# Kernel optimization log

Hardware: AMD Instinct MI355X
Metric: run time of the kernel (lower is better)

The kernel has to match this reference:

```python
import jax, jax.numpy as jnp
import numpy as np

N = 50000      # nodes
E = 800000     # edges (avg degree 16)
IN = 128       # in_dim == hidden_dim*num_heads so residuals fire
D = 32         # hidden_dim (per-head)
H = 4          # num_heads
OUT = 64       # out_dim (final layer has 1 head)
NEG_SLOPE = 0.2
LN_EPS = 1e-5


def setup_inputs() -> dict:
    key = jax.random.key(0)
    ks = jax.random.split(key, 16)
    rn = lambda k, s: jax.random.normal(k, s, jnp.float32) * 0.05
    return {
        "features": jax.random.normal(ks[0], (N, IN), jnp.float32),
        "edge_weight": jax.random.uniform(ks[1], (E,), jnp.float32),
        "src": jax.random.randint(ks[2], (E,), 0, N),
        "dst": jax.random.randint(ks[3], (E,), 0, N),
        "W0": rn(ks[4], (IN, H * D)), "al0": rn(ks[5], (H, D)), "ar0": rn(ks[6], (H, D)), "lam0": jnp.float32(1.0),
        "W1": rn(ks[7], (H * D, H * D)), "al1": rn(ks[8], (H, D)), "ar1": rn(ks[9], (H, D)), "lam1": jnp.float32(1.0),
        "W2": rn(ks[10], (H * D, OUT)), "al2": rn(ks[11], (1, OUT)), "ar2": rn(ks[12], (1, OUT)), "lam2": jnp.float32(1.0),
        "g0": jnp.ones((H * D,), jnp.float32), "b0": jnp.zeros((H * D,), jnp.float32),
        "g1": jnp.ones((H * D,), jnp.float32), "b1": jnp.zeros((H * D,), jnp.float32),
    }


def _gat_layer(h, W, al, ar, lam, src, dst, ew):
    n = h.shape[0]
    heads, d = al.shape
    ft = (h @ W).reshape(n, heads, d)                      # [N,H,D]
    el = jnp.sum(ft * al[None], axis=-1)                   # [N,H]
    er = jnp.sum(ft * ar[None], axis=-1)                   # [N,H]
    e = el[src] + er[dst] + lam * ew[:, None]              # [E,H] u_add_v + weight bias
    e = jax.nn.leaky_relu(e, NEG_SLOPE)
    # edge softmax over incoming edges of each dst node
    m = jax.ops.segment_max(e, dst, num_segments=n)        # [N,H]
    ex = jnp.exp(e - m[dst])
    s = jax.ops.segment_sum(ex, dst, num_segments=n)       # [N,H]
    a = ex / s[dst]                                        # [E,H]
    # u_mul_e + sum aggregation
    msg = ft[src] * a[:, :, None]                          # [E,H,D]
    return jax.ops.segment_sum(msg, dst, num_segments=n)   # [N,H,D]


def _layer_norm(x, g, b):
    mu = jnp.mean(x, axis=-1, keepdims=True)
    var = jnp.mean((x - mu) ** 2, axis=-1, keepdims=True)
    return (x - mu) * jax.lax.rsqrt(var + LN_EPS) * g + b


def _forward(features, edge_weight, src, dst,
             W0, al0, ar0, lam0, W1, al1, ar1, lam1, W2, al2, ar2, lam2,
             g0, b0, g1, b1):
    n = features.shape[0]
    h = features
    # layer 0
    h1 = _gat_layer(h, W0, al0, ar0, lam0, src, dst, edge_weight)
    h1 = jax.nn.elu(h1).reshape(n, -1)
    h1 = _layer_norm(h1, g0, b0)
    if h1.shape == h.shape:
        h1 = h1 + h
    # layer 1
    h2 = _gat_layer(h1, W1, al1, ar1, lam1, src, dst, edge_weight)
    h2 = jax.nn.elu(h2).reshape(n, -1)
    h2 = _layer_norm(h2, g1, b1)
    h2 = h2 + h1
    # layer 2 (single head, no activation)
    out = _gat_layer(h2, W2, al2, ar2, lam2, src, dst, edge_weight).reshape(n, -1)
    return out


def reference(features, edge_weight, src, dst,
              W0, al0, ar0, lam0, W1, al1, ar1, lam1, W2, al2, ar2, lam2,
              g0, b0, g1, b1):
    # eval mode: dropout off and _add_noise is identity, so noisy == clean
    h_clean = _forward(features, edge_weight, src, dst,
                       W0, al0, ar0, lam0, W1, al1, ar1, lam1, W2, al2, ar2, lam2,
                       g0, b0, g1, b1)
    return (h_clean, h_clean)
```

## Files before the change

### kernel.cpp

```cpp
#include <hip/hip_runtime.h>

#define NEG_SLOPE 0.2f
#define LN_EPS 1e-5f

typedef __attribute__((ext_vector_type(8))) short bf16x8;
typedef __attribute__((ext_vector_type(4))) float f32x4;

__device__ inline unsigned short f2bf(float f) {
    unsigned u = __float_as_uint(f);
    unsigned r = u + 0x7FFFu + ((u >> 16) & 1u);
    return (unsigned short)(r >> 16);
}

__device__ inline void unpack8(uint4 u, float* f) {
    f[0] = __uint_as_float(u.x << 16);
    f[1] = __uint_as_float(u.x & 0xFFFF0000u);
    f[2] = __uint_as_float(u.y << 16);
    f[3] = __uint_as_float(u.y & 0xFFFF0000u);
    f[4] = __uint_as_float(u.z << 16);
    f[5] = __uint_as_float(u.z & 0xFFFF0000u);
    f[6] = __uint_as_float(u.w << 16);
    f[7] = __uint_as_float(u.w & 0xFFFF0000u);
}


__global__ void prep_kernel(const int* __restrict__ dst, int* __restrict__ counts,
                            int* __restrict__ rank, int E, int RB,
                            const float* __restrict__ W0, const float* __restrict__ W1,
                            const float* __restrict__ W2, unsigned short* __restrict__ Wt0,
                            unsigned short* __restrict__ Wt1,
                            unsigned short* __restrict__ Wt2) {
    int bid = blockIdx.x;
    if (bid < RB) {
        int i = bid * 256 + threadIdx.x;
        if (i < E) rank[i] = atomicAdd(&counts[dst[i] * 16], 1);
    } else {
        int row = (bid - RB) * 2 + (threadIdx.x >> 7);
        int k = threadIdx.x & 127;
        if (row < 128) {
            Wt0[row * 128 + k] = f2bf(W0[k * 128 + row]);
        } else if (row < 256) {
            int c = row - 128;
            Wt1[c * 128 + k] = f2bf(W1[k * 128 + c]);
        } else {
            int c = row - 256;
            Wt2[c * 128 + k] = f2bf(W2[k * 64 + c]);
        }
    }
}

__global__ __launch_bounds__(256) void scan1_kernel(const int* __restrict__ counts,
                                                    int* __restrict__ bsum,
                                                    int* __restrict__ dhist, int n) {
    __shared__ int lds[256];
    __shared__ int hbin[64];
    int t = threadIdx.x;
    if (t < 64) hbin[t] = 0;
    int i = blockIdx.x * 256 + t;
    int c = (i < n) ? counts[i * 16] : 0;
    lds[t] = c;
    __syncthreads();
    if (i < n) atomicAdd(&hbin[63 - (c < 63 ? c : 63)], 1);
    for (int off = 128; off > 0; off >>= 1) {
        int v = (t < off) ? lds[t + off] : 0;
        __syncthreads();
        if (t < off) lds[t] += v;
        __syncthreads();
    }
    if (t == 0) bsum[blockIdx.x] = lds[0];
    if (t < 64) {
        int h = hbin[t];
        if (h) atomicAdd(&dhist[t], h);
    }
}

__global__ __launch_bounds__(256) void scan3_kernel(const int* __restrict__ counts,
                                                    const int* __restrict__ bsum,
                                                    int* __restrict__ rowptr,
                                                    const int* __restrict__ dhist,
                                                    int* __restrict__ dbase,
                                                    int n, int E, int nscan) {
    __shared__ int lds[256];
    int t = threadIdx.x;
    lds[t] = (t < nscan) ? bsum[t] : 0;
    __syncthreads();
    for (int off = 1; off < 256; off <<= 1) {
        int v = (t >= off) ? lds[t - off] : 0;
        __syncthreads();
        lds[t] += v;
        __syncthreads();
    }
    int boff = (blockIdx.x > 0) ? lds[blockIdx.x - 1] : 0;
    __syncthreads();
    int i = blockIdx.x * 256 + t;
    int c = (i < n) ? counts[i * 16] : 0;
    lds[t] = c;
    __syncthreads();
    for (int off = 1; off < 256; off <<= 1) {
        int v = (t >= off) ? lds[t - off] : 0;
        __syncthreads();
        lds[t] += v;
        __syncthreads();
    }
    if (i < n) rowptr[i] = boff + lds[t] - c;
    if (i == n) rowptr[n] = E;
    if (blockIdx.x == 0 && t < 64) {
        int v = dhist[t];
        int x = v;
        #pragma unroll
        for (int off = 1; off < 64; off <<= 1) {
            int u = __shfl_up(x, off, 64);
            if (t >= off) x += u;
        }
        dbase[t] = x - v;
    }
}

__global__ __launch_bounds__(256) void place_kernel(
    const int* __restrict__ src, const int* __restrict__ dst,
    const float* __restrict__ ew, const int* __restrict__ rowptr,
    const int* __restrict__ rank, unsigned* __restrict__ edge_p,
    const int* __restrict__ dbase, int* __restrict__ dcount,
    int* __restrict__ perm, int E, int EB, int N) {
    __shared__ int lbin[64];
    __shared__ int lbase[64];
    int bid = blockIdx.x;
    int t = threadIdx.x;
    if (bid < EB) {
        int i = bid * 256 + t;
        if (i < E) {
            int p = rowptr[dst[i]] + rank[i];
            edge_p[p] = ((unsigned)f2bf(ew[i]) << 16) | (unsigned)src[i];
        }
    } else {
        if (t < 64) lbin[t] = 0;
        __syncthreads();
        int nidx = (bid - EB) * 256 + t;
        bool valid = nidx < N;
        int key = 0, myoff = 0;
        if (valid) {
            int deg = rowptr[nidx + 1] - rowptr[nidx];
            key = 63 - (deg < 63 ? deg : 63);
            myoff = atomicAdd(&lbin[key], 1);
        }
        __syncthreads();
        if (t < 64) lbase[t] = lbin[t] ? atomicAdd(&dcount[t], lbin[t]) : 0;
        __syncthreads();
        if (valid) perm[dbase[key] + lbase[key] + myoff] = nidx;
    }
}


template <int NT, int H, bool A32>
__global__ __launch_bounds__(256) void gemm_mfma(const void* __restrict__ Ap,
                                                 const unsigned short* __restrict__ Wt,
                                                 const float* __restrict__ al,
                                                 const float* __restrict__ ar,
                                                 unsigned short* __restrict__ ftb,
                                                 float* __restrict__ el,
                                                 float* __restrict__ er, int n) {
    constexpr int LDA = 136;
    constexpr int D = NT * 16 / H;
    __shared__ unsigned short As[64 * LDA];
    __shared__ unsigned short Ws[NT * 16 * LDA];
    int t = threadIdx.x;
    int row0 = blockIdx.x * 64;

    if constexpr (A32) {
        const float4* A4 = (const float4*)Ap;
        #pragma unroll
        for (int j = 0; j < 8; ++j) {
            int idx = t + j * 256;
            int r = idx >> 5;
            int c4 = idx & 31;
            int row = row0 + r;
            float4 v = (row < n) ? A4[(size_t)row * 32 + c4] : make_float4(0.f, 0.f, 0.f, 0.f);
            unsigned p0 = (unsigned)f2bf(v.x) | ((unsigned)f2bf(v.y) << 16);
            unsigned p1 = (unsigned)f2bf(v.z) | ((unsigned)f2bf(v.w) << 16);
            *(uint2*)&As[r * LDA + c4 * 4] = make_uint2(p0, p1);
        }
    } else {
        const uint4* A16 = (const uint4*)Ap;
        #pragma unroll
        for (int j = 0; j < 4; ++j) {
            int idx = t + j * 256;
            int r = idx >> 4;
            int c8 = idx & 15;
            int row = row0 + r;
            uint4 v = (row < n) ? A16[(size_t)row * 16 + c8] : make_uint4(0, 0, 0, 0);
            *(uint4*)&As[r * LDA + c8 * 8] = v;
        }
    }
    const uint4* Wg = (const uint4*)Wt;
    #pragma unroll
    for (int j = 0; j < NT; ++j) {
        int idx = t + j * 256;
        int r = idx >> 4;
        int c8 = idx & 15;
        *(uint4*)&Ws[r * LDA + c8 * 8] = Wg[idx];
    }
    __syncthreads();

    int w = t >> 6, lane = t & 63;
    int m = lane & 15, q = lane >> 4;
    f32x4 acc[NT] = {};
    const unsigned short* ap = &As[(w * 16 + m) * LDA + q * 8];
    #pragma unroll
    for (int kk = 0; kk < 4; ++kk) {
        bf16x8 a = *(const bf16x8*)(ap + kk * 32);
        #pragma unroll
        for (int nt = 0; nt < NT; ++nt) {
            bf16x8 b = *(const bf16x8*)&Ws[(nt * 16 + m) * LDA + kk * 32 + q * 8];
            acc[nt] = __builtin_amdgcn_mfma_f32_16x16x32_bf16(a, b, acc[nt], 0, 0, 0);
        }
    }

    float alv[NT], arv[NT];
    #pragma unroll
    for (int nt = 0; nt < NT; ++nt) {
        alv[nt] = al[nt * 16 + m];
        arv[nt] = ar[nt * 16 + m];
    }

    int orow = row0 + w * 16 + q * 4;
    #pragma unroll
    for (int r = 0; r < 4; ++r) {
        int row = orow + r;
        float pl[H] = {}, pr[H] = {};
        #pragma unroll
        for (int nt = 0; nt < NT; ++nt) {
            int h = (nt * 16) / D;
            pl[h] = fmaf(acc[nt][r], alv[nt], pl[h]);
            pr[h] = fmaf(acc[nt][r], arv[nt], pr[h]);
        }
        #pragma unroll
        for (int off = 1; off < 16; off <<= 1) {
            #pragma unroll
            for (int h = 0; h < H; ++h) {
                pl[h] += __shfl_xor(pl[h], off, 64);
                pr[h] += __shfl_xor(pr[h], off, 64);
            }
        }
        if (row < n) {
            #pragma unroll
            for (int nt = 0; nt < NT; ++nt)
                ftb[(size_t)row * (NT * 16) + nt * 16 + m] = f2bf(acc[nt][r]);
            if (m < H) {
                float vl = pl[0], vr = pr[0];
                #pragma unroll
                for (int h = 1; h < H; ++h)
                    if (m == h) { vl = pl[h]; vr = pr[h]; }
                el[row * H + m] = vl;
                er[row * H + m] = vr;
            }
        }
    }
}


__device__ inline void accum8(float* ax, uint4 u, float p) {
    ax[0] = fmaf(p, __uint_as_float(u.x << 16), ax[0]);
    ax[1] = fmaf(p, __uint_as_float(u.x & 0xFFFF0000u), ax[1]);
    ax[2] = fmaf(p, __uint_as_float(u.y << 16), ax[2]);
    ax[3] = fmaf(p, __uint_as_float(u.y & 0xFFFF0000u), ax[3]);
    ax[4] = fmaf(p, __uint_as_float(u.z << 16), ax[4]);
    ax[5] = fmaf(p, __uint_as_float(u.z & 0xFFFF0000u), ax[5]);
    ax[6] = fmaf(p, __uint_as_float(u.w << 16), ax[6]);
    ax[7] = fmaf(p, __uint_as_float(u.w & 0xFFFF0000u), ax[7]);
}

__device__ inline void accum4(float* ax, uint2 u, float p) {
    ax[0] = fmaf(p, __uint_as_float(u.x << 16), ax[0]);
    ax[1] = fmaf(p, __uint_as_float(u.x & 0xFFFF0000u), ax[1]);
    ax[2] = fmaf(p, __uint_as_float(u.y << 16), ax[2]);
    ax[3] = fmaf(p, __uint_as_float(u.y & 0xFFFF0000u), ax[3]);
}

template <int K>
__device__ inline void agg_batch(const uint4* __restrict__ ftb4,
                                 const float* __restrict__ el, unsigned ev, int j,
                                 int li, int head, float erv, float lam, float* ax,
                                 float& s) {
    unsigned ee[K];
    uint4 uu[K];
    float ll[K];
    #pragma unroll
    for (int k = 0; k < K; ++k) ee[k] = __shfl(ev, j + k, 16);
    #pragma unroll
    for (int k = 0; k < K; ++k) {
        unsigned sn = ee[k] & 0xFFFFu;
        uu[k] = ftb4[(size_t)sn * 16 + li];
        ll[k] = el[sn * 4 + head];
    }
    #pragma unroll
    for (int k = 0; k < K; ++k) {
        float v = ll[k] + erv + lam * __uint_as_float(ee[k] & 0xFFFF0000u);
        v = fmaxf(v, NEG_SLOPE * v);
        float p = __expf(v);
        accum8(ax, uu[k], p);
        s += p;
    }
}

template <int K>
__device__ inline void agg_batch_out(const uint2* __restrict__ ftb2,
                                     const float* __restrict__ el, unsigned ev,
                                     int j, int li, float erv, float lam, float* ax,
                                     float& s) {
    unsigned ee[K];
    uint2 uu[K];
    float ll[K];
    #pragma unroll
    for (int k = 0; k < K; ++k) ee[k] = __shfl(ev, j + k, 16);
    #pragma unroll
    for (int k = 0; k < K; ++k) {
        unsigned sn = ee[k] & 0xFFFFu;
        uu[k] = ftb2[(size_t)sn * 16 + li];
        ll[k] = el[sn];
    }
    #pragma unroll
    for (int k = 0; k < K; ++k) {
        float v = ll[k] + erv + lam * __uint_as_float(ee[k] & 0xFFFF0000u);
        v = fmaxf(v, NEG_SLOPE * v);
        float p = __expf(v);
        accum4(ax, uu[k], p);
        s += p;
    }
}

template <bool PREV32>
__global__ __launch_bounds__(256) void gat_agg_ln(
    const int* __restrict__ rowptr, const unsigned* __restrict__ edge_p,
    const int* __restrict__ perm, const uint4* __restrict__ ftb4,
    const float* __restrict__ el, const float* __restrict__ er,
    const float* __restrict__ lam_p, const float* __restrict__ g,
    const float* __restrict__ b, const void* __restrict__ prevp,
    uint4* __restrict__ outb, int n) {
    int gid = blockIdx.x * 16 + (threadIdx.x >> 4);
    if (gid >= n) return;
    int node = perm[gid];
    int li = threadIdx.x & 15;
    int head = li >> 2;
    float lam = lam_p[0];
    float erv = er[node * 4 + head];
    int s0 = rowptr[node], s1 = rowptr[node + 1];
    float ax[8] = {};
    float s = 0.f;

    for (int base = s0; base < s1; base += 16) {
        int m = s1 - base;
        if (m > 16) m = 16;
        unsigned ev = (li < m) ? edge_p[base + li] : 0u;
        int j = 0;
        for (; j + 8 <= m; j += 8)
            agg_batch<8>(ftb4, el, ev, j, li, head, erv, lam, ax, s);
        if (j + 4 <= m) {
            agg_batch<4>(ftb4, el, ev, j, li, head, erv, lam, ax, s);
            j += 4;
        }
        for (; j < m; ++j)
            agg_batch<1>(ftb4, el, ev, j, li, head, erv, lam, ax, s);
    }

    float inv = (s > 0.f) ? 1.f / s : 0.f;
    float x[8];
    float sum = 0.f, sq = 0.f;
    #pragma unroll
    for (int d = 0; d < 8; ++d) {
        float v = ax[d] * inv;
        v = (v > 0.f) ? v : expm1f(v);
        x[d] = v;
        sum += v;
        sq += v * v;
    }
    #pragma unroll
    for (int off = 1; off < 16; off <<= 1) {
        sum += __shfl_xor(sum, off, 16);
        sq += __shfl_xor(sq, off, 16);
    }
    float mu = sum * (1.f / 128.f);
    float var = sq * (1.f / 128.f) - mu * mu;
    float rs = rsqrtf(var + LN_EPS);

    const float4* g4 = (const float4*)g;
    const float4* b4 = (const float4*)b;
    float pv[8];
    if constexpr (PREV32) {
        const float4* p4 = (const float4*)prevp;
        #pragma unroll
        for (int h = 0; h < 2; ++h) {
            float4 v = p4[(size_t)node * 32 + li * 2 + h];
            pv[h * 4 + 0] = v.x; pv[h * 4 + 1] = v.y;
            pv[h * 4 + 2] = v.z; pv[h * 4 + 3] = v.w;
        }
    } else {
        unpack8(((const uint4*)prevp)[(size_t)node * 16 + li], pv);
    }
    float y[8];
    #pragma unroll
    for (int h = 0; h < 2; ++h) {
        float4 gv = g4[li * 2 + h];
        float4 bv = b4[li * 2 + h];
        y[h * 4 + 0] = (x[h * 4 + 0] - mu) * rs * gv.x + bv.x + pv[h * 4 + 0];
        y[h * 4 + 1] = (x[h * 4 + 1] - mu) * rs * gv.y + bv.y + pv[h * 4 + 1];
        y[h * 4 + 2] = (x[h * 4 + 2] - mu) * rs * gv.z + bv.z + pv[h * 4 + 2];
        y[h * 4 + 3] = (x[h * 4 + 3] - mu) * rs * gv.w + bv.w + pv[h * 4 + 3];
    }
    uint4 o;
    o.x = (unsigned)f2bf(y[0]) | ((unsigned)f2bf(y[1]) << 16);
    o.y = (unsigned)f2bf(y[2]) | ((unsigned)f2bf(y[3]) << 16);
    o.z = (unsigned)f2bf(y[4]) | ((unsigned)f2bf(y[5]) << 16);
    o.w = (unsigned)f2bf(y[6]) | ((unsigned)f2bf(y[7]) << 16);
    outb[(size_t)node * 16 + li] = o;
}

__global__ __launch_bounds__(256) void gat_agg_out(
    const int* __restrict__ rowptr, const unsigned* __restrict__ edge_p,
    const int* __restrict__ perm, const uint2* __restrict__ ftb2,
    const float* __restrict__ el, const float* __restrict__ er,
    const float* __restrict__ lam_p, float* __restrict__ out, int n) {
    int gid = blockIdx.x * 16 + (threadIdx.x >> 4);
    if (gid >= n) return;
    int node = perm[gid];
    int li = threadIdx.x & 15;
    float lam = lam_p[0];
    float erv = er[node];
    int s0 = rowptr[node], s1 = rowptr[node + 1];
    float ax[4] = {};
    float s = 0.f;

    for (int base = s0; base < s1; base += 16) {
        int m = s1 - base;
        if (m > 16) m = 16;
        unsigned ev = (li < m) ? edge_p[base + li] : 0u;
        int j = 0;
        for (; j + 8 <= m; j += 8)
            agg_batch_out<8>(ftb2, el, ev, j, li, erv, lam, ax, s);
        if (j + 4 <= m) {
            agg_batch_out<4>(ftb2, el, ev, j, li, erv, lam, ax, s);
            j += 4;
        }
        for (; j < m; ++j)
            agg_batch_out<1>(ftb2, el, ev, j, li, erv, lam, ax, s);
    }

    float inv = (s > 0.f) ? 1.f / s : 0.f;
    float4 y;
    y.x = ax[0] * inv;
    y.y = ax[1] * inv;
    y.z = ax[2] * inv;
    y.w = ax[3] * inv;
    ((float4*)out)[(size_t)node * 16 + li] = y;
    ((float4*)out)[(size_t)(n + node) * 16 + li] = y;
}


extern "C" void kernel_launch(void* const* d_in, const int* in_sizes, int n_in,
                              void* d_out, int out_size, void* d_ws, size_t ws_size,
                              hipStream_t stream) {
    const float* features = (const float*)d_in[0];
    const float* edge_weight = (const float*)d_in[1];
    const int* src = (const int*)d_in[2];
    const int* dst = (const int*)d_in[3];
    const float* W0 = (const float*)d_in[4];
    const float* al0 = (const float*)d_in[5];
    const float* ar0 = (const float*)d_in[6];
    const float* lam0 = (const float*)d_in[7];
    const float* W1 = (const float*)d_in[8];
    const float* al1 = (const float*)d_in[9];
    const float* ar1 = (const float*)d_in[10];
    const float* lam1 = (const float*)d_in[11];
    const float* W2 = (const float*)d_in[12];
    const float* al2 = (const float*)d_in[13];
    const float* ar2 = (const float*)d_in[14];
    const float* lam2 = (const float*)d_in[15];
    const float* g0 = (const float*)d_in[16];
    const float* b0 = (const float*)d_in[17];
    const float* g1 = (const float*)d_in[18];
    const float* b1 = (const float*)d_in[19];

    const int N = in_sizes[0] / 128;
    const int E = in_sizes[1];

    char* w = (char*)d_ws;
    size_t o = 0;
    auto carve = [&](size_t bytes) {
        char* p = w + o;
        o += (bytes + 255) & ~(size_t)255;
        return p;
    };
    int* counts = (int*)carve((size_t)N * 64);
    int* dhist = (int*)carve(256);
    int* dcount = (int*)carve(256);
    int* rowptr = (int*)carve((size_t)(N + 1) * 4);
    int* bsum = (int*)carve(256 * 4);
    int* rank = (int*)carve((size_t)E * 4);
    unsigned* edge_p = (unsigned*)carve((size_t)E * 4);
    int* dbase = (int*)carve(256);
    int* perm = (int*)carve((size_t)N * 4);
    unsigned short* ftb = (unsigned short*)carve((size_t)N * 128 * 2);
    unsigned short* h1 = (unsigned short*)carve((size_t)N * 128 * 2);
    unsigned short* h2 = (unsigned short*)carve((size_t)N * 128 * 2);
    float* el = (float*)carve((size_t)N * 4 * 4);
    float* er = (float*)carve((size_t)N * 4 * 4);
    unsigned short* Wt0 = (unsigned short*)carve(128 * 128 * 2);
    unsigned short* Wt1 = (unsigned short*)carve(128 * 128 * 2);
    unsigned short* Wt2 = (unsigned short*)carve(64 * 128 * 2);

    const int nscan = (N + 255) / 256;
    const int ngemm = (N + 63) / 64;
    const int nagg = (N + 15) / 16;
    const int RB = (E + 255) / 256;

    hipMemsetAsync(counts, 0, (size_t)N * 64 + 512, stream);
    prep_kernel<<<RB + 160, 256, 0, stream>>>(dst, counts, rank, E, RB,
                                              W0, W1, W2, Wt0, Wt1, Wt2);
    scan1_kernel<<<nscan, 256, 0, stream>>>(counts, bsum, dhist, N);
    scan3_kernel<<<(N + 1 + 255) / 256, 256, 0, stream>>>(counts, bsum, rowptr,
                                                          dhist, dbase, N, E, nscan);
    place_kernel<<<RB + nscan, 256, 0, stream>>>(src, dst, edge_weight, rowptr, rank,
                                                 edge_p, dbase, dcount, perm, E, RB, N);

    gemm_mfma<8, 4, true><<<ngemm, 256, 0, stream>>>(features, Wt0, al0, ar0,
                                                     ftb, el, er, N);
    gat_agg_ln<true><<<nagg, 256, 0, stream>>>(rowptr, edge_p, perm, (const uint4*)ftb,
                                               el, er, lam0, g0, b0, features,
                                               (uint4*)h1, N);
    gemm_mfma<8, 4, false><<<ngemm, 256, 0, stream>>>(h1, Wt1, al1, ar1, ftb, el, er, N);
    gat_agg_ln<false><<<nagg, 256, 0, stream>>>(rowptr, edge_p, perm, (const uint4*)ftb,
                                                el, er, lam1, g1, b1, h1, (uint4*)h2, N);
    gemm_mfma<4, 1, false><<<ngemm, 256, 0, stream>>>(h2, Wt2, al2, ar2, ftb, el, er, N);
    gat_agg_out<<<nagg, 256, 0, stream>>>(rowptr, edge_p, perm, (const uint2*)ftb,
                                          el, er, lam2, (float*)d_out, N);
}
```

Measured before the change: 294.5 us.

## Fuse aggregation with next-layer GEMM and merge histogram with first GEMM

Each aggregation+LayerNorm kernel now also does the next layer's MFMA projection and attention logits on its 16-node tile, so the h2 round trip and the separate GEMM launches go away. The first GEMM shares a launch with the dst-degree histogram. The degree-sorted node permutation is dropped, and counts are zeroed by a custom kernel instead of a memset. This cuts launches and global traffic, but the fused kernels read weights straight from global per wave, and losing degree sorting may worsen load balance.

```diff
diff --git a/kernel.cpp b/kernel.cpp
--- a/kernel.cpp
+++ b/kernel.cpp
@@ -24,18 +24,21 @@
 }
 
 
-__global__ void prep_kernel(const int* __restrict__ dst, int* __restrict__ counts,
-                            int* __restrict__ rank, int E, int RB,
-                            const float* __restrict__ W0, const float* __restrict__ W1,
-                            const float* __restrict__ W2, unsigned short* __restrict__ Wt0,
-                            unsigned short* __restrict__ Wt1,
-                            unsigned short* __restrict__ Wt2) {
+__global__ __launch_bounds__(256) void zero_wt_kernel(
+    uint4* __restrict__ z, int nz, int ZB,
+    const float* __restrict__ W0, const float* __restrict__ W1,
+    const float* __restrict__ W2, unsigned short* __restrict__ Wt0,
+    unsigned short* __restrict__ Wt1, unsigned short* __restrict__ Wt2) {
     int bid = blockIdx.x;
-    if (bid < RB) {
-        int i = bid * 256 + threadIdx.x;
-        if (i < E) rank[i] = atomicAdd(&counts[dst[i] * 16], 1);
+    if (bid < ZB) {
+        int base = bid * 1024 + threadIdx.x;
+        #pragma unroll
+        for (int j = 0; j < 4; ++j) {
+            int idx = base + j * 256;
+            if (idx < nz) z[idx] = make_uint4(0, 0, 0, 0);
+        }
     } else {
-        int row = (bid - RB) * 2 + (threadIdx.x >> 7);
+        int row = (bid - ZB) * 2 + (threadIdx.x >> 7);
         int k = threadIdx.x & 127;
         if (row < 128) {
             Wt0[row * 128 + k] = f2bf(W0[k * 128 + row]);
@@ -49,18 +52,111 @@
     }
 }
 
+
+__global__ __launch_bounds__(256) void hist_gemm0(
+    const int* __restrict__ dst, int* __restrict__ counts, int* __restrict__ rank,
+    int E, int RB, const float* __restrict__ Ap, const unsigned short* __restrict__ Wt,
+    const float* __restrict__ al, const float* __restrict__ ar,
+    unsigned short* __restrict__ ftb, float* __restrict__ el,
+    float* __restrict__ er, int n) {
+    constexpr int LDA = 136;
+    constexpr int NT = 8, H = 4, D = 32;
+    __shared__ unsigned short As[64 * LDA];
+    __shared__ unsigned short Ws[NT * 16 * LDA];
+    int t = threadIdx.x;
+    if (blockIdx.x < RB) {
+        int i = blockIdx.x * 256 + t;
+        if (i < E) rank[i] = atomicAdd(&counts[dst[i] * 16], 1);
+        return;
+    }
+    int row0 = (blockIdx.x - RB) * 64;
+
+    const float4* A4 = (const float4*)Ap;
+    #pragma unroll
+    for (int j = 0; j < 8; ++j) {
+        int idx = t + j * 256;
+        int r = idx >> 5;
+        int c4 = idx & 31;
+        int row = row0 + r;
+        float4 v = (row < n) ? A4[(size_t)row * 32 + c4] : make_float4(0.f, 0.f, 0.f, 0.f);
+        unsigned p0 = (unsigned)f2bf(v.x) | ((unsigned)f2bf(v.y) << 16);
+        unsigned p1 = (unsigned)f2bf(v.z) | ((unsigned)f2bf(v.w) << 16);
+        *(uint2*)&As[r * LDA + c4 * 4] = make_uint2(p0, p1);
+    }
+    const uint4* Wg = (const uint4*)Wt;
+    #pragma unroll
+    for (int j = 0; j < NT; ++j) {
+        int idx = t + j * 256;
+        int r = idx >> 4;
+        int c8 = idx & 15;
+        *(uint4*)&Ws[r * LDA + c8 * 8] = Wg[idx];
+    }
+    __syncthreads();
+
+    int w = t >> 6, lane = t & 63;
+    int m = lane & 15, q = lane >> 4;
+    f32x4 acc[NT] = {};
+    const unsigned short* ap = &As[(w * 16 + m) * LDA + q * 8];
+    #pragma unroll
+    for (int kk = 0; kk < 4; ++kk) {
+        bf16x8 a = *(const bf16x8*)(ap + kk * 32);
+        #pragma unroll
+        for (int nt = 0; nt < NT; ++nt) {
+            bf16x8 b = *(const bf16x8*)&Ws[(nt * 16 + m) * LDA + kk * 32 + q * 8];
+            acc[nt] = __builtin_amdgcn_mfma_f32_16x16x32_bf16(a, b, acc[nt], 0, 0, 0);
+        }
+    }
+
+    float alv[NT], arv[NT];
+    #pragma unroll
+    for (int nt = 0; nt < NT; ++nt) {
+        alv[nt] = al[nt * 16 + m];
+        arv[nt] = ar[nt * 16 + m];
+    }
+
+    int orow = row0 + w * 16 + q * 4;
+    #pragma unroll
+    for (int r = 0; r < 4; ++r) {
+        int row = orow + r;
+        float pl[H] = {}, pr[H] = {};
+        #pragma unroll
+        for (int nt = 0; nt < NT; ++nt) {
+            int h = (nt * 16) / D;
+            pl[h] = fmaf(acc[nt][r], alv[nt], pl[h]);
+            pr[h] = fmaf(acc[nt][r], arv[nt], pr[h]);
+        }
+        #pragma unroll
+        for (int off = 1; off < 16; off <<= 1) {
+            #pragma unroll
+            for (int h = 0; h < H; ++h) {
+                pl[h] += __shfl_xor(pl[h], off, 64);
+                pr[h] += __shfl_xor(pr[h], off, 64);
+            }
+        }
+        if (row < n) {
+            #pragma unroll
+            for (int nt = 0; nt < NT; ++nt)
+                ftb[(size_t)row * 128 + nt * 16 + m] = f2bf(acc[nt][r]);
+            if (m < H) {
+                float vl = pl[0], vr = pr[0];
+                #pragma unroll
+                for (int h = 1; h < H; ++h)
+                    if (m == h) { vl = pl[h]; vr = pr[h]; }
+                el[row * H + m] = vl;
+                er[row * H + m] = vr;
+            }
+        }
+    }
+}
+
+
 __global__ __launch_bounds__(256) void scan1_kernel(const int* __restrict__ counts,
-                                                    int* __restrict__ bsum,
-                                                    int* __restrict__ dhist, int n) {
+                                                    int* __restrict__ bsum, int n) {
     __shared__ int lds[256];
-    __shared__ int hbin[64];
     int t = threadIdx.x;
-    if (t < 64) hbin[t] = 0;
     int i = blockIdx.x * 256 + t;
-    int c = (i < n) ? counts[i * 16] : 0;
-    lds[t] = c;
+    lds[t] = (i < n) ? counts[i * 16] : 0;
     __syncthreads();
-    if (i < n) atomicAdd(&hbin[63 - (c < 63 ? c : 63)], 1);
     for (int off = 128; off > 0; off >>= 1) {
         int v = (t < off) ? lds[t + off] : 0;
         __syncthreads();
@@ -68,18 +164,13 @@
         __syncthreads();
     }
     if (t == 0) bsum[blockIdx.x] = lds[0];
-    if (t < 64) {
-        int h = hbin[t];
-        if (h) atomicAdd(&dhist[t], h);
-    }
-}
+}
+
 
 __global__ __launch_bounds__(256) void scan3_kernel(const int* __restrict__ counts,
                                                     const int* __restrict__ bsum,
-                                                    int* __restrict__ rowptr,
-                                                    const int* __restrict__ dhist,
-                                                    int* __restrict__ dbase,
-                                                    int n, int E, int nscan) {
+                                                    int* __restrict__ rowptr, int n,
+                                                    int E, int nscan) {
     __shared__ int lds[256];
     int t = threadIdx.x;
     lds[t] = (t < nscan) ? bsum[t] : 0;
@@ -104,156 +195,17 @@
     }
     if (i < n) rowptr[i] = boff + lds[t] - c;
     if (i == n) rowptr[n] = E;
-    if (blockIdx.x == 0 && t < 64) {
-        int v = dhist[t];
-        int x = v;
-        #pragma unroll
-        for (int off = 1; off < 64; off <<= 1) {
-            int u = __shfl_up(x, off, 64);
-            if (t >= off) x += u;
-        }
-        dbase[t] = x - v;
-    }
-}
+}
+
 
 __global__ __launch_bounds__(256) void place_kernel(
     const int* __restrict__ src, const int* __restrict__ dst,
     const float* __restrict__ ew, const int* __restrict__ rowptr,
-    const int* __restrict__ rank, unsigned* __restrict__ edge_p,
-    const int* __restrict__ dbase, int* __restrict__ dcount,
-    int* __restrict__ perm, int E, int EB, int N) {
-    __shared__ int lbin[64];
-    __shared__ int lbase[64];
-    int bid = blockIdx.x;
-    int t = threadIdx.x;
-    if (bid < EB) {
-        int i = bid * 256 + t;
-        if (i < E) {
-            int p = rowptr[dst[i]] + rank[i];
-            edge_p[p] = ((unsigned)f2bf(ew[i]) << 16) | (unsigned)src[i];
-        }
-    } else {
-        if (t < 64) lbin[t] = 0;
-        __syncthreads();
-        int nidx = (bid - EB) * 256 + t;
-        bool valid = nidx < N;
-        int key = 0, myoff = 0;
-        if (valid) {
-            int deg = rowptr[nidx + 1] - rowptr[nidx];
-            key = 63 - (deg < 63 ? deg : 63);
-            myoff = atomicAdd(&lbin[key], 1);
-        }
-        __syncthreads();
-        if (t < 64) lbase[t] = lbin[t] ? atomicAdd(&dcount[t], lbin[t]) : 0;
-        __syncthreads();
-        if (valid) perm[dbase[key] + lbase[key] + myoff] = nidx;
-    }
-}
-
-
-template <int NT, int H, bool A32>
-__global__ __launch_bounds__(256) void gemm_mfma(const void* __restrict__ Ap,
-                                                 const unsigned short* __restrict__ Wt,
-                                                 const float* __restrict__ al,
-                                                 const float* __restrict__ ar,
-                                                 unsigned short* __restrict__ ftb,
-                                                 float* __restrict__ el,
-                                                 float* __restrict__ er, int n) {
-    constexpr int LDA = 136;
-    constexpr int D = NT * 16 / H;
-    __shared__ unsigned short As[64 * LDA];
-    __shared__ unsigned short Ws[NT * 16 * LDA];
-    int t = threadIdx.x;
-    int row0 = blockIdx.x * 64;
-
-    if constexpr (A32) {
-        const float4* A4 = (const float4*)Ap;
-        #pragma unroll
-        for (int j = 0; j < 8; ++j) {
-            int idx = t + j * 256;
-            int r = idx >> 5;
-            int c4 = idx & 31;
-            int row = row0 + r;
-            float4 v = (row < n) ? A4[(size_t)row * 32 + c4] : make_float4(0.f, 0.f, 0.f, 0.f);
-            unsigned p0 = (unsigned)f2bf(v.x) | ((unsigned)f2bf(v.y) << 16);
-            unsigned p1 = (unsigned)f2bf(v.z) | ((unsigned)f2bf(v.w) << 16);
-            *(uint2*)&As[r * LDA + c4 * 4] = make_uint2(p0, p1);
-        }
-    } else {
-        const uint4* A16 = (const uint4*)Ap;
-        #pragma unroll
-        for (int j = 0; j < 4; ++j) {
-            int idx = t + j * 256;
-            int r = idx >> 4;
-            int c8 = idx & 15;
-            int row = row0 + r;
-            uint4 v = (row < n) ? A16[(size_t)row * 16 + c8] : make_uint4(0, 0, 0, 0);
-            *(uint4*)&As[r * LDA + c8 * 8] = v;
-        }
-    }
-    const uint4* Wg = (const uint4*)Wt;
-    #pragma unroll
-    for (int j = 0; j < NT; ++j) {
-        int idx = t + j * 256;
-        int r = idx >> 4;
-        int c8 = idx & 15;
-        *(uint4*)&Ws[r * LDA + c8 * 8] = Wg[idx];
-    }
-    __syncthreads();
-
-    int w = t >> 6, lane = t & 63;
-    int m = lane & 15, q = lane >> 4;
-    f32x4 acc[NT] = {};
-    const unsigned short* ap = &As[(w * 16 + m) * LDA + q * 8];
-    #pragma unroll
-    for (int kk = 0; kk < 4; ++kk) {
-        bf16x8 a = *(const bf16x8*)(ap + kk * 32);
-        #pragma unroll
-        for (int nt = 0; nt < NT; ++nt) {
-            bf16x8 b = *(const bf16x8*)&Ws[(nt * 16 + m) * LDA + kk * 32 + q * 8];
-            acc[nt] = __builtin_amdgcn_mfma_f32_16x16x32_bf16(a, b, acc[nt], 0, 0, 0);
-        }
-    }
-
-    float alv[NT], arv[NT];
-    #pragma unroll
-    for (int nt = 0; nt < NT; ++nt) {
-        alv[nt] = al[nt * 16 + m];
-        arv[nt] = ar[nt * 16 + m];
-    }
-
-    int orow = row0 + w * 16 + q * 4;
-    #pragma unroll
-    for (int r = 0; r < 4; ++r) {
-        int row = orow + r;
-        float pl[H] = {}, pr[H] = {};
-        #pragma unroll
-        for (int nt = 0; nt < NT; ++nt) {
-            int h = (nt * 16) / D;
-            pl[h] = fmaf(acc[nt][r], alv[nt], pl[h]);
-            pr[h] = fmaf(acc[nt][r], arv[nt], pr[h]);
-        }
-        #pragma unroll
-        for (int off = 1; off < 16; off <<= 1) {
-            #pragma unroll
-            for (int h = 0; h < H; ++h) {
-                pl[h] += __shfl_xor(pl[h], off, 64);
-                pr[h] += __shfl_xor(pr[h], off, 64);
-            }
-        }
-        if (row < n) {
-            #pragma unroll
-            for (int nt = 0; nt < NT; ++nt)
-                ftb[(size_t)row * (NT * 16) + nt * 16 + m] = f2bf(acc[nt][r]);
-            if (m < H) {
-                float vl = pl[0], vr = pr[0];
-                #pragma unroll
-                for (int h = 1; h < H; ++h)
-                    if (m == h) { vl = pl[h]; vr = pr[h]; }
-                el[row * H + m] = vl;
-                er[row * H + m] = vr;
-            }
-        }
+    const int* __restrict__ rank, unsigned* __restrict__ edge_p, int E) {
+    int i = blockIdx.x * 256 + threadIdx.x;
+    if (i < E) {
+        int p = rowptr[dst[i]] + rank[i];
+        edge_p[p] = ((unsigned)f2bf(ew[i]) << 16) | (unsigned)src[i];
     }
 }
 
@@ -328,100 +280,185 @@
     }
 }
 
-template <bool PREV32>
-__global__ __launch_bounds__(256) void gat_agg_ln(
+
+template <bool PREV32, int VER>
+__global__ __launch_bounds__(256) void fused_agg_gemm(
     const int* __restrict__ rowptr, const unsigned* __restrict__ edge_p,
-    const int* __restrict__ perm, const uint4* __restrict__ ftb4,
-    const float* __restrict__ el, const float* __restrict__ er,
-    const float* __restrict__ lam_p, const float* __restrict__ g,
-    const float* __restrict__ b, const void* __restrict__ prevp,
-    uint4* __restrict__ outb, int n) {
-    int gid = blockIdx.x * 16 + (threadIdx.x >> 4);
-    if (gid >= n) return;
-    int node = perm[gid];
-    int li = threadIdx.x & 15;
-    int head = li >> 2;
-    float lam = lam_p[0];
-    float erv = er[node * 4 + head];
-    int s0 = rowptr[node], s1 = rowptr[node + 1];
-    float ax[8] = {};
-    float s = 0.f;
-
-    for (int base = s0; base < s1; base += 16) {
-        int m = s1 - base;
-        if (m > 16) m = 16;
-        unsigned ev = (li < m) ? edge_p[base + li] : 0u;
-        int j = 0;
-        for (; j + 8 <= m; j += 8)
-            agg_batch<8>(ftb4, el, ev, j, li, head, erv, lam, ax, s);
-        if (j + 4 <= m) {
-            agg_batch<4>(ftb4, el, ev, j, li, head, erv, lam, ax, s);
-            j += 4;
-        }
-        for (; j < m; ++j)
-            agg_batch<1>(ftb4, el, ev, j, li, head, erv, lam, ax, s);
-    }
-
-    float inv = (s > 0.f) ? 1.f / s : 0.f;
-    float x[8];
-    float sum = 0.f, sq = 0.f;
-    #pragma unroll
-    for (int d = 0; d < 8; ++d) {
-        float v = ax[d] * inv;
-        v = (v > 0.f) ? v : expm1f(v);
-        x[d] = v;
-        sum += v;
-        sq += v * v;
-    }
-    #pragma unroll
-    for (int off = 1; off < 16; off <<= 1) {
-        sum += __shfl_xor(sum, off, 16);
-        sq += __shfl_xor(sq, off, 16);
-    }
-    float mu = sum * (1.f / 128.f);
-    float var = sq * (1.f / 128.f) - mu * mu;
-    float rs = rsqrtf(var + LN_EPS);
-
-    const float4* g4 = (const float4*)g;
-    const float4* b4 = (const float4*)b;
-    float pv[8];
-    if constexpr (PREV32) {
-        const float4* p4 = (const float4*)prevp;
+    const uint4* __restrict__ ftb4, const float* __restrict__ el_in,
+    const float* __restrict__ er_in, const float* __restrict__ lam_p,
+    const float* __restrict__ g, const float* __restrict__ b,
+    const void* __restrict__ prevp, uint4* __restrict__ houtb,
+    const unsigned short* __restrict__ Wt, const float* __restrict__ al,
+    const float* __restrict__ ar, unsigned short* __restrict__ ftb_out,
+    float* __restrict__ el_out, float* __restrict__ er_out, int n) {
+    constexpr int LDA = 136;
+    __shared__ unsigned short As[16 * LDA];
+    __shared__ float red[2][4][16];
+    int t = threadIdx.x;
+    int node0 = blockIdx.x * 16;
+    int nl = t >> 4;
+    int node = node0 + nl;
+    int li = t & 15;
+
+    if (node < n) {
+        int head = li >> 2;
+        float lam = lam_p[0];
+        float erv = er_in[node * 4 + head];
+        int s0 = rowptr[node], s1 = rowptr[node + 1];
+        float ax[8] = {};
+        float s = 0.f;
+
+        for (int base = s0; base < s1; base += 16) {
+            int m = s1 - base;
+            if (m > 16) m = 16;
+            unsigned ev = (li < m) ? edge_p[base + li] : 0u;
+            int j = 0;
+            for (; j + 8 <= m; j += 8)
+                agg_batch<8>(ftb4, el_in, ev, j, li, head, erv, lam, ax, s);
+            if (j + 4 <= m) {
+                agg_batch<4>(ftb4, el_in, ev, j, li, head, erv, lam, ax, s);
+                j += 4;
+            }
+            for (; j < m; ++j)
+                agg_batch<1>(ftb4, el_in, ev, j, li, head, erv, lam, ax, s);
+        }
+
+        float inv = (s > 0.f) ? 1.f / s : 0.f;
+        float x[8];
+        float sum = 0.f, sq = 0.f;
+        #pragma unroll
+        for (int d = 0; d < 8; ++d) {
+            float v = ax[d] * inv;
+            v = (v > 0.f) ? v : expm1f(v);
+            x[d] = v;
+            sum += v;
+            sq += v * v;
+        }
+        #pragma unroll
+        for (int off = 1; off < 16; off <<= 1) {
+            sum += __shfl_xor(sum, off, 16);
+            sq += __shfl_xor(sq, off, 16);
+        }
+        float mu = sum * (1.f / 128.f);
+        float var = sq * (1.f / 128.f) - mu * mu;
+        float rs = rsqrtf(var + LN_EPS);
+
+        const float4* g4 = (const float4*)g;
+        const float4* b4 = (const float4*)b;
+        float pv[8];
+        if constexpr (PREV32) {
+            const float4* p4 = (const float4*)prevp;
+            #pragma unroll
+            for (int h = 0; h < 2; ++h) {
+                float4 v = p4[(size_t)node * 32 + li * 2 + h];
+                pv[h * 4 + 0] = v.x; pv[h * 4 + 1] = v.y;
+                pv[h * 4 + 2] = v.z; pv[h * 4 + 3] = v.w;
+            }
+        } else {
+            unpack8(((const uint4*)prevp)[(size_t)node * 16 + li], pv);
+        }
+        float y[8];
         #pragma unroll
         for (int h = 0; h < 2; ++h) {
-            float4 v = p4[(size_t)node * 32 + li * 2 + h];
-            pv[h * 4 + 0] = v.x; pv[h * 4 + 1] = v.y;
-            pv[h * 4 + 2] = v.z; pv[h * 4 + 3] = v.w;
-        }
+            float4 gv = g4[li * 2 + h];
+            float4 bv = b4[li * 2 + h];
+            y[h * 4 + 0] = (x[h * 4 + 0] - mu) * rs * gv.x + bv.x + pv[h * 4 + 0];
+            y[h * 4 + 1] = (x[h * 4 + 1] - mu) * rs * gv.y + bv.y + pv[h * 4 + 1];
+            y[h * 4 + 2] = (x[h * 4 + 2] - mu) * rs * gv.z + bv.z + pv[h * 4 + 2];
+            y[h * 4 + 3] = (x[h * 4 + 3] - mu) * rs * gv.w + bv.w + pv[h * 4 + 3];
+        }
+        uint4 o;
+        o.x = (unsigned)f2bf(y[0]) | ((unsigned)f2bf(y[1]) << 16);
+        o.y = (unsigned)f2bf(y[2]) | ((unsigned)f2bf(y[3]) << 16);
+        o.z = (unsigned)f2bf(y[4]) | ((unsigned)f2bf(y[5]) << 16);
+        o.w = (unsigned)f2bf(y[6]) | ((unsigned)f2bf(y[7]) << 16);
+        if constexpr (VER == 1) houtb[(size_t)node * 16 + li] = o;
+        *(uint4*)&As[nl * LDA + li * 8] = o;
     } else {
-        unpack8(((const uint4*)prevp)[(size_t)node * 16 + li], pv);
-    }
-    float y[8];
-    #pragma unroll
-    for (int h = 0; h < 2; ++h) {
-        float4 gv = g4[li * 2 + h];
-        float4 bv = b4[li * 2 + h];
-        y[h * 4 + 0] = (x[h * 4 + 0] - mu) * rs * gv.x + bv.x + pv[h * 4 + 0];
-        y[h * 4 + 1] = (x[h * 4 + 1] - mu) * rs * gv.y + bv.y + pv[h * 4 + 1];
-        y[h * 4 + 2] = (x[h * 4 + 2] - mu) * rs * gv.z + bv.z + pv[h * 4 + 2];
-        y[h * 4 + 3] = (x[h * 4 + 3] - mu) * rs * gv.w + bv.w + pv[h * 4 + 3];
-    }
-    uint4 o;
-    o.x = (unsigned)f2bf(y[0]) | ((unsigned)f2bf(y[1]) << 16);
-    o.y = (unsigned)f2bf(y[2]) | ((unsigned)f2bf(y[3]) << 16);
-    o.z = (unsigned)f2bf(y[4]) | ((unsigned)f2bf(y[5]) << 16);
-    o.w = (unsigned)f2bf(y[6]) | ((unsigned)f2bf(y[7]) << 16);
-    outb[(size_t)node * 16 + li] = o;
-}
+        *(uint4*)&As[nl * LDA + li * 8] = make_uint4(0, 0, 0, 0);
+    }
+    __syncthreads();
+
+    int w = t >> 6, lane = t & 63;
+    int m = lane & 15, q = lane >> 4;
+    if constexpr (VER == 1) {
+        f32x4 acc[2] = {};
+        #pragma unroll
+        for (int kk = 0; kk < 4; ++kk) {
+            bf16x8 a = *(const bf16x8*)&As[m * LDA + kk * 32 + q * 8];
+            #pragma unroll
+            for (int nt = 0; nt < 2; ++nt) {
+                int col = w * 32 + nt * 16 + m;
+                bf16x8 bb = *(const bf16x8*)&Wt[(size_t)col * 128 + kk * 32 + q * 8];
+                acc[nt] = __builtin_amdgcn_mfma_f32_16x16x32_bf16(a, bb, acc[nt], 0, 0, 0);
+            }
+        }
+        float alv0 = al[w * 32 + m], alv1 = al[w * 32 + 16 + m];
+        float arv0 = ar[w * 32 + m], arv1 = ar[w * 32 + 16 + m];
+        #pragma unroll
+        for (int r = 0; r < 4; ++r) {
+            int row = node0 + q * 4 + r;
+            float pl = acc[0][r] * alv0 + acc[1][r] * alv1;
+            float pr = acc[0][r] * arv0 + acc[1][r] * arv1;
+            #pragma unroll
+            for (int off = 1; off < 16; off <<= 1) {
+                pl += __shfl_xor(pl, off, 64);
+                pr += __shfl_xor(pr, off, 64);
+            }
+            if (row < n) {
+                ftb_out[(size_t)row * 128 + w * 32 + m] = f2bf(acc[0][r]);
+                ftb_out[(size_t)row * 128 + w * 32 + 16 + m] = f2bf(acc[1][r]);
+                if (m == 0) {
+                    el_out[row * 4 + w] = pl;
+                    er_out[row * 4 + w] = pr;
+                }
+            }
+        }
+    } else {
+        f32x4 acc = {};
+        #pragma unroll
+        for (int kk = 0; kk < 4; ++kk) {
+            bf16x8 a = *(const bf16x8*)&As[m * LDA + kk * 32 + q * 8];
+            int col = w * 16 + m;
+            bf16x8 bb = *(const bf16x8*)&Wt[(size_t)col * 128 + kk * 32 + q * 8];
+            acc = __builtin_amdgcn_mfma_f32_16x16x32_bf16(a, bb, acc, 0, 0, 0);
+        }
+        float alv = al[w * 16 + m], arv = ar[w * 16 + m];
+        #pragma unroll
+        for (int r = 0; r < 4; ++r) {
+            int row = node0 + q * 4 + r;
+            float pl = acc[r] * alv;
+            float pr = acc[r] * arv;
+            #pragma unroll
+            for (int off = 1; off < 16; off <<= 1) {
+                pl += __shfl_xor(pl, off, 64);
+                pr += __shfl_xor(pr, off, 64);
+            }
+            if (row < n) ftb_out[(size_t)row * 64 + w * 16 + m] = f2bf(acc[r]);
+            if (m == 0) {
+                red[0][w][q * 4 + r] = pl;
+                red[1][w][q * 4 + r] = pr;
+            }
+        }
+        __syncthreads();
+        if (t < 16) {
+            int row = node0 + t;
+            if (row < n) {
+                el_out[row] = red[0][0][t] + red[0][1][t] + red[0][2][t] + red[0][3][t];
+                er_out[row] = red[1][0][t] + red[1][1][t] + red[1][2][t] + red[1][3][t];
+            }
+        }
+    }
+}
+
 
 __global__ __launch_bounds__(256) void gat_agg_out(
     const int* __restrict__ rowptr, const unsigned* __restrict__ edge_p,
-    const int* __restrict__ perm, const uint2* __restrict__ ftb2,
-    const float* __restrict__ el, const float* __restrict__ er,
-    const float* __restrict__ lam_p, float* __restrict__ out, int n) {
-    int gid = blockIdx.x * 16 + (threadIdx.x >> 4);
-    if (gid >= n) return;
-    int node = perm[gid];
+    const uint2* __restrict__ ftb2, const float* __restrict__ el,
+    const float* __restrict__ er, const float* __restrict__ lam_p,
+    float* __restrict__ out, int n) {
+    int node = blockIdx.x * 16 + (threadIdx.x >> 4);
+    if (node >= n) return;
     int li = threadIdx.x & 15;
     float lam = lam_p[0];
     float erv = er[node];
@@ -490,19 +527,20 @@
         return p;
     };
     int* counts = (int*)carve((size_t)N * 64);
-    int* dhist = (int*)carve(256);
-    int* dcount = (int*)carve(256);
     int* rowptr = (int*)carve((size_t)(N + 1) * 4);
     int* bsum = (int*)carve(256 * 4);
     int* rank = (int*)carve((size_t)E * 4);
     unsigned* edge_p = (unsigned*)carve((size_t)E * 4);
-    int* dbase = (int*)carve(256);
-    int* perm = (int*)carve((size_t)N * 4);
-    unsigned short* ftb = (unsigned short*)carve((size_t)N * 128 * 2);
+    unsigned short* ftbA = (unsigned short*)carve((size_t)N * 128 * 2);
+    unsigned short* ftbB = (unsigned short*)carve((size_t)N * 128 * 2);
+    unsigned short* ftbC = (unsigned short*)carve((size_t)N * 64 * 2);
     unsigned short* h1 = (unsigned short*)carve((size_t)N * 128 * 2);
-    unsigned short* h2 = (unsigned short*)carve((size_t)N * 128 * 2);
-    float* el = (float*)carve((size_t)N * 4 * 4);
-    float* er = (float*)carve((size_t)N * 4 * 4);
+    float* elA = (float*)carve((size_t)N * 4 * 4);
+    float* erA = (float*)carve((size_t)N * 4 * 4);
+    float* elB = (float*)carve((size_t)N * 4 * 4);
+    float* erB = (float*)carve((size_t)N * 4 * 4);
+    float* elC = (float*)carve((size_t)N * 4);
+    float* erC = (float*)carve((size_t)N * 4);
     unsigned short* Wt0 = (unsigned short*)carve(128 * 128 * 2);
     unsigned short* Wt1 = (unsigned short*)carve(128 * 128 * 2);
     unsigned short* Wt2 = (unsigned short*)carve(64 * 128 * 2);
@@ -511,25 +549,25 @@
     const int ngemm = (N + 63) / 64;
     const int nagg = (N + 15) / 16;
     const int RB = (E + 255) / 256;
-
-    hipMemsetAsync(counts, 0, (size_t)N * 64 + 512, stream);
-    prep_kernel<<<RB + 160, 256, 0, stream>>>(dst, counts, rank, E, RB,
-                                              W0, W1, W2, Wt0, Wt1, Wt2);
-    scan1_kernel<<<nscan, 256, 0, stream>>>(counts, bsum, dhist, N);
-    scan3_kernel<<<(N + 1 + 255) / 256, 256, 0, stream>>>(counts, bsum, rowptr,
-                                                          dhist, dbase, N, E, nscan);
-    place_kernel<<<RB + nscan, 256, 0, stream>>>(src, dst, edge_weight, rowptr, rank,
-                                                 edge_p, dbase, dcount, perm, E, RB, N);
-
-    gemm_mfma<8, 4, true><<<ngemm, 256, 0, stream>>>(features, Wt0, al0, ar0,
-                                                     ftb, el, er, N);
-    gat_agg_ln<true><<<nagg, 256, 0, stream>>>(rowptr, edge_p, perm, (const uint4*)ftb,
-                                               el, er, lam0, g0, b0, features,
-                                               (uint4*)h1, N);
-    gemm_mfma<8, 4, false><<<ngemm, 256, 0, stream>>>(h1, Wt1, al1, ar1, ftb, el, er, N);
-    gat_agg_ln<false><<<nagg, 256, 0, stream>>>(rowptr, edge_p, perm, (const uint4*)ftb,
-                                                el, er, lam1, g1, b1, h1, (uint4*)h2, N);
-    gemm_mfma<4, 1, false><<<ngemm, 256, 0, stream>>>(h2, Wt2, al2, ar2, ftb, el, er, N);
-    gat_agg_out<<<nagg, 256, 0, stream>>>(rowptr, edge_p, perm, (const uint2*)ftb,
-                                          el, er, lam2, (float*)d_out, N);
-}
+    const int nz = N * 4;
+    const int ZB = (nz + 1023) / 1024;
+
+    zero_wt_kernel<<<ZB + 160, 256, 0, stream>>>((uint4*)counts, nz, ZB,
+                                                 W0, W1, W2, Wt0, Wt1, Wt2);
+    hist_gemm0<<<RB + ngemm, 256, 0, stream>>>(dst, counts, rank, E, RB,
+                                               features, Wt0, al0, ar0,
+                                               ftbA, elA, erA, N);
+    scan1_kernel<<<nscan, 256, 0, stream>>>(counts, bsum, N);
+    scan3_kernel<<<(N + 1 + 255) / 256, 256, 0, stream>>>(counts, bsum, rowptr, N, E,
+                                                          nscan);
+    place_kernel<<<RB, 256, 0, stream>>>(src, dst, edge_weight, rowptr, rank,
+                                         edge_p, E);
+    fused_agg_gemm<true, 1><<<nagg, 256, 0, stream>>>(
+        rowptr, edge_p, (const uint4*)ftbA, elA, erA, lam0, g0, b0, features,
+        (uint4*)h1, Wt1, al1, ar1, ftbB, elB, erB, N);
+    fused_agg_gemm<false, 2><<<nagg, 256, 0, stream>>>(
+        rowptr, edge_p, (const uint4*)ftbB, elB, erB, lam1, g1, b1, h1,
+        nullptr, Wt2, al2, ar2, ftbC, elC, erC, N);
+    gat_agg_out<<<nagg, 256, 0, stream>>>(rowptr, edge_p, (const uint2*)ftbC,
+                                          elC, erC, lam2, (float*)d_out, N);
+}
```

After: 295.8 us. No clear change (+0.4%).
